# Kernel optimization log

Hardware: AMD Instinct MI355X
Metric: run time of the kernel (lower is better)

## Reference

```python
import jax, jax.numpy as jnp
import numpy as np

N_HEADS = 16
ROPE_BASE = 10000.0


def _rope_cos_sin(seq_len, head_dim, dtype):
    half = head_dim // 2
    inv_freq = 1.0 / (ROPE_BASE ** (jnp.arange(0, half, dtype=jnp.float32) / half))
    ang = jnp.arange(seq_len, dtype=jnp.float32)[:, None] * inv_freq[None, :]  # [S, half]
    cos = jnp.concatenate([jnp.cos(ang), jnp.cos(ang)], axis=-1).astype(dtype)  # [S, hd]
    sin = jnp.concatenate([jnp.sin(ang), jnp.sin(ang)], axis=-1).astype(dtype)
    return cos, sin


def _rotate_half(x):
    half = x.shape[-1] // 2
    return jnp.concatenate([-x[..., half:], x[..., :half]], axis=-1)


def setup_inputs() -> dict:
    key = jax.random.key(0)
    k1, k2, k3 = jax.random.split(key, 3)
    B, S, D = 2, 2048, 1024
    x = jax.random.normal(k1, (B, S, D), dtype=jnp.float32)
    w_qkv = jax.random.normal(k2, (D, 3 * D), dtype=jnp.float32) * (1.0 / np.sqrt(D))
    w_out = jax.random.normal(k3, (D, D), dtype=jnp.float32) * (1.0 / np.sqrt(D))
    return {"x": x, "w_qkv": w_qkv, "w_out": w_out}


def reference(x, w_qkv, w_out):
    B, S, D = x.shape
    H = N_HEADS
    hd = D // H
    scale = 1.0 / np.sqrt(hd)

    qkv = x @ w_qkv  # [B, S, 3D]
    q, k, v = jnp.split(qkv, 3, axis=-1)
    # [B, H, S, hd]
    q = q.reshape(B, S, H, hd).transpose(0, 2, 1, 3)
    k = k.reshape(B, S, H, hd).transpose(0, 2, 1, 3)
    v = v.reshape(B, S, H, hd).transpose(0, 2, 1, 3)

    cos, sin = _rope_cos_sin(S, hd, x.dtype)  # [S, hd]
    q = q * cos + _rotate_half(q) * sin
    k = k * cos + _rotate_half(k) * sin

    scores = jnp.einsum("bhqd,bhkd->bhqk", q, k) * scale  # [B, H, S, S]
    causal = jnp.tril(jnp.ones((S, S), dtype=bool))
    scores = jnp.where(causal[None, None, :, :], scores, -jnp.inf)

    probs = jax.nn.softmax(scores.astype(jnp.float32), axis=-1).astype(q.dtype)
    out = jnp.einsum("bhqk,bhkd->bhqd", probs, v)  # [B, H, S, hd]
    out = out.transpose(0, 2, 1, 3).reshape(B, S, D)
    return out @ w_out
```

## Files before the change

### kernel.cpp

```cpp
#include <hip/hip_runtime.h>
#include <math.h>
#include <type_traits>

#define B_  2
#define S_  2048
#define D_  1024
#define H_  16

typedef short bf16x8 __attribute__((ext_vector_type(8)));
typedef short bf16x4 __attribute__((ext_vector_type(4)));
typedef float f32x4  __attribute__((ext_vector_type(4)));

__device__ __forceinline__ short f2bf(float f) {
    unsigned u = __builtin_bit_cast(unsigned, f);
    u += 0x7FFFu + ((u >> 16) & 1u);
    return (short)(u >> 16);
}
__device__ __forceinline__ float bf2f(short s) {
    unsigned u = ((unsigned)(unsigned short)s) << 16;
    return __builtin_bit_cast(float, u);
}

__device__ __forceinline__ void gload16(const short* g, const void* l) {
    __builtin_amdgcn_global_load_lds(
        (const __attribute__((address_space(1))) void*)g,
        (__attribute__((address_space(3))) void*)l, 16, 0, 0);
}

__device__ __forceinline__ void transpose_body(
    const float* __restrict__ in, short* __restrict__ out, int K, int N,
    int bx, int by, short (*t)[72], int tid)
{
    const int k0 = by * 64, n0 = bx * 64;
    const int r = tid >> 2;
    const int c = (tid & 3) * 16;
    const float* src = in + (size_t)(k0 + r) * N + n0 + c;
#pragma unroll
    for (int i = 0; i < 16; ++i) t[c + i][r] = f2bf(src[i]);
    __syncthreads();
    short* dst = out + (size_t)(n0 + r) * K + k0 + c;
    *(bf16x8*)(dst)     = *(const bf16x8*)&t[r][c];
    *(bf16x8*)(dst + 8) = *(const bf16x8*)&t[r][c + 8];
}

__global__ __launch_bounds__(256) void prep_kernel(
    const float* __restrict__ x, short* __restrict__ Xb,
    const float* __restrict__ w_qkv, short* __restrict__ Wqt,
    const float* __restrict__ w_out, short* __restrict__ Wot,
    float2* __restrict__ tab)
{
    __shared__ short t[64][72];
    const int bid = blockIdx.x;
    const int tid = threadIdx.x;
    if (bid < 2048) {
        int i = (bid * 256 + tid) * 8;
        float4 a = *(const float4*)(x + i);
        float4 b = *(const float4*)(x + i + 4);
        bf16x8 o;
        o[0] = f2bf(a.x); o[1] = f2bf(a.y); o[2] = f2bf(a.z); o[3] = f2bf(a.w);
        o[4] = f2bf(b.x); o[5] = f2bf(b.y); o[6] = f2bf(b.z); o[7] = f2bf(b.w);
        *(bf16x8*)(Xb + i) = o;
    } else if (bid < 2816) {
        int b2 = bid - 2048;
        transpose_body(w_qkv, Wqt, 1024, 3072, b2 % 48, b2 / 48, t, tid);
    } else if (bid < 3072) {
        int b2 = bid - 2816;
        transpose_body(w_out, Wot, 1024, 1024, b2 % 16, b2 / 16, t, tid);
    } else {
        int idx = (bid - 3072) * 256 + tid;
        int j = idx & 31, s = idx >> 5;
        float inv = powf(10000.0f, -(float)j * (1.0f / 32.0f));
        float sn, cs;
        sincosf((float)s * inv, &sn, &cs);
        tab[idx] = make_float2(cs, sn);
    }
}

__global__ __launch_bounds__(256) void gemm_bt_f32(
    const short* __restrict__ A, const short* __restrict__ Bt,
    float* __restrict__ C, int M, int N, int K)
{
    __shared__ short smem[18432];

    const int tid  = threadIdx.x;
    const int wave = tid >> 6, lane = tid & 63;
    const int quad = lane >> 4, l16 = lane & 15;
    const int wm = wave >> 1, wn = wave & 1;

    const int nbx = N >> 6;
    const int cpx = gridDim.x >> 3;
    const int lin = blockIdx.x;
    const int swz = (lin & 7) * cpx + (lin >> 3);
    const int row0 = (swz / nbx) * 128, col0 = (swz % nbx) * 64;

    f32x4 acc[4][2];
#pragma unroll
    for (int mi = 0; mi < 4; ++mi)
#pragma unroll
        for (int ni = 0; ni < 2; ++ni) acc[mi][ni] = (f32x4)0.f;

    const int sr = tid >> 2;
    const int sc = (tid & 3) * 8;
    const short* a0 = A  + (size_t)(row0 + sr) * K + sc;
    const short* a1 = A  + (size_t)(row0 + 64 + sr) * K + sc;
    const short* b0 = Bt + (size_t)(col0 + sr) * K + sc;

    auto stage = [&](int b, int kt) {
        char* l = (char*)(smem + b * 6144) + wave * 1024;
        const int k0 = kt * 32;
        gload16(a0 + k0, l);
        gload16(a1 + k0, l + 4096);
        gload16(b0 + k0, l + 8192);
    };

    const int NT = K >> 5;
    stage(0, 0);
    stage(1, 1);
    int bufid = 0;
    for (int kt = 0; kt < NT; ++kt) {
        if (kt + 1 < NT) { asm volatile("s_waitcnt vmcnt(3)" ::: "memory"); }
        else             { asm volatile("s_waitcnt vmcnt(0)" ::: "memory"); }
        __builtin_amdgcn_s_barrier();
        __builtin_amdgcn_sched_barrier(0);
        if (kt + 2 < NT) {
            int nb = bufid + 2; if (nb >= 3) nb -= 3;
            stage(nb, kt + 2);
        }

        const short* As = smem + bufid * 6144;
        const short* Bs = As + 4096;
        bf16x8 af[4], bfr[2];
#pragma unroll
        for (int mi = 0; mi < 4; ++mi)
            af[mi] = *(const bf16x8*)(As + (wm * 64 + mi * 16 + l16) * 32 + quad * 8);
#pragma unroll
        for (int ni = 0; ni < 2; ++ni)
            bfr[ni] = *(const bf16x8*)(Bs + (wn * 32 + ni * 16 + l16) * 32 + quad * 8);
#pragma unroll
        for (int mi = 0; mi < 4; ++mi)
#pragma unroll
            for (int ni = 0; ni < 2; ++ni)
                acc[mi][ni] = __builtin_amdgcn_mfma_f32_16x16x32_bf16(
                    af[mi], bfr[ni], acc[mi][ni], 0, 0, 0);

        bufid = (bufid + 1 == 3) ? 0 : bufid + 1;
    }

#pragma unroll
    for (int mi = 0; mi < 4; ++mi)
#pragma unroll
        for (int ni = 0; ni < 2; ++ni)
#pragma unroll
            for (int r = 0; r < 4; ++r) {
                int row = row0 + wm * 64 + mi * 16 + quad * 4 + r;
                int col = col0 + wn * 32 + ni * 16 + l16;
                C[(size_t)row * N + col] = acc[mi][ni][r];
            }
}

__global__ __launch_bounds__(256) void gemm_qkv(
    const short* __restrict__ A, const short* __restrict__ Bt,
    const float2* __restrict__ tab,
    short* __restrict__ Qb, short* __restrict__ Kb, short* __restrict__ Vt)
{
    const int K = 1024;
    extern __shared__ short smem[];
    short* Sc = smem;

    const int tid  = threadIdx.x;
    const int wave = tid >> 6, lane = tid & 63;
    const int quad = lane >> 4, l16 = lane & 15;
    const int wm = wave >> 1, wn = wave & 1;

    const int lin = blockIdx.x;
    const int swz = (lin & 7) * 96 + (lin >> 3);
    const int row0 = (swz / 24) * 128, col0 = (swz % 24) * 128;

    f32x4 acc[4][4];
#pragma unroll
    for (int mi = 0; mi < 4; ++mi)
#pragma unroll
        for (int ni = 0; ni < 4; ++ni) acc[mi][ni] = (f32x4)0.f;

    const int sr = tid >> 2;
    const int sc = (tid & 3) * 8;
    const short* a0 = A  + (size_t)(row0 + sr) * K + sc;
    const short* a1 = A  + (size_t)(row0 + 64 + sr) * K + sc;
    const short* b0 = Bt + (size_t)(col0 + sr) * K + sc;
    const short* b1 = Bt + (size_t)(col0 + 64 + sr) * K + sc;

    auto stage = [&](int b, int kt) {
        char* l = (char*)(smem + b * 8192) + wave * 1024;
        const int k0 = kt * 32;
        gload16(a0 + k0, l);
        gload16(a1 + k0, l + 4096);
        gload16(b0 + k0, l + 8192);
        gload16(b1 + k0, l + 12288);
    };

    const int NT = K >> 5;
    stage(0, 0);
    stage(1, 1);
    int bufid = 0;
    for (int kt = 0; kt < NT; ++kt) {
        if (kt + 1 < NT) { asm volatile("s_waitcnt vmcnt(4)" ::: "memory"); }
        else             { asm volatile("s_waitcnt vmcnt(0)" ::: "memory"); }
        __builtin_amdgcn_s_barrier();
        __builtin_amdgcn_sched_barrier(0);
        if (kt + 2 < NT) {
            int nb = bufid + 2; if (nb >= 3) nb -= 3;
            stage(nb, kt + 2);
        }

        const short* As = smem + bufid * 8192;
        const short* Bs = As + 4096;
        bf16x8 af[4], bfr[4];
#pragma unroll
        for (int mi = 0; mi < 4; ++mi)
            af[mi] = *(const bf16x8*)(As + (wm * 64 + mi * 16 + l16) * 32 + quad * 8);
#pragma unroll
        for (int ni = 0; ni < 4; ++ni)
            bfr[ni] = *(const bf16x8*)(Bs + (wn * 64 + ni * 16 + l16) * 32 + quad * 8);
#pragma unroll
        for (int mi = 0; mi < 4; ++mi)
#pragma unroll
            for (int ni = 0; ni < 4; ++ni)
                acc[mi][ni] = __builtin_amdgcn_mfma_f32_16x16x32_bf16(
                    af[mi], bfr[ni], acc[mi][ni], 0, 0, 0);

        bufid = (bufid + 1 == 3) ? 0 : bufid + 1;
    }

    __syncthreads();

    const int sec  = (col0 + wn * 64) >> 6;
    const int h    = sec & 15;
    const int kind = sec >> 4;
    short* myS = Sc + wave * 4608;

    const int mrow0 = row0 + wm * 64;
    const int b  = mrow0 >> 11;
    const int bh = b * 16 + h;
    const int sbase = mrow0 & (S_ - 1);

    if (kind < 2) {
#pragma unroll
        for (int mi = 0; mi < 4; ++mi) {
#pragma unroll
            for (int r = 0; r < 4; ++r) {
                int sl = mi * 16 + quad * 4 + r;
                int s = sbase + sl;
#pragma unroll
                for (int ni = 0; ni < 2; ++ni) {
                    int j = ni * 16 + l16;
                    float2 t = tab[s * 32 + j];
                    float lo = acc[mi][ni][r], hi = acc[mi][ni + 2][r];
                    float olo = lo * t.x - hi * t.y;
                    float ohi = hi * t.x + lo * t.y;
                    if (kind == 0) { olo *= 0.125f; ohi *= 0.125f; }
                    myS[sl * 72 + j]      = f2bf(olo);
                    myS[sl * 72 + 32 + j] = f2bf(ohi);
                }
            }
        }
        const int rl = lane >> 3;
        const int cl = (lane & 7) * 8;
        short* dst = (kind == 0 ? Qb : Kb);
#pragma unroll
        for (int p = 0; p < 8; ++p) {
            int rr = p * 8 + rl;
            bf16x8 v = *(const bf16x8*)&myS[rr * 72 + cl];
            *(bf16x8*)(dst + ((size_t)bh * S_ + sbase + rr) * 64 + cl) = v;
        }
    } else {
#pragma unroll
        for (int mi = 0; mi < 4; ++mi)
#pragma unroll
            for (int ni = 0; ni < 4; ++ni) {
                bf16x4 p;
                p[0] = f2bf(acc[mi][ni][0]);
                p[1] = f2bf(acc[mi][ni][1]);
                p[2] = f2bf(acc[mi][ni][2]);
                p[3] = f2bf(acc[mi][ni][3]);
                *(bf16x4*)&myS[(ni * 16 + l16) * 72 + mi * 16 + quad * 4] = p;
            }
        const int rl = lane >> 3;
        const int cl = (lane & 7) * 8;
#pragma unroll
        for (int p = 0; p < 8; ++p) {
            int dd = p * 8 + rl;
            bf16x8 v = *(const bf16x8*)&myS[dd * 72 + cl];
            *(bf16x8*)(Vt + ((size_t)bh * 64 + dd) * S_ + sbase + cl) = v;
        }
    }
}

__global__ __launch_bounds__(256, 3) void attn_kernel(
    const short* __restrict__ Qb, const short* __restrict__ Kb,
    const short* __restrict__ Vt, short* __restrict__ Opart,
    float* __restrict__ lpart)
{
    __shared__ short Ks[2][64 * 64];
    __shared__ short Vs[2][64 * 64];
    __shared__ short Ps[128][72];

    const int lin = blockIdx.x;
    const int xcd = lin & 7;
    const int j   = lin >> 3;
    const int bh   = xcd * 4 + (j & 3);
    const int task = j >> 2;

    const int g = task < 4 ? 0 : task < 12 ? 1 : task < 24 ? 2 : 3;
    const int cumstart = g == 0 ? 0 : g == 1 ? 4 : g == 2 ? 12 : 24;
    const int idx = task - cumstart;
    const int qd = idx / (g + 1);
    const int qb = 4 * g + qd;
    const int c  = idx - qd * (g + 1);
    const int t0 = c * 8;
    const int t1 = min(2 * qb + 1, c * 8 + 7);

    const int wave = threadIdx.x >> 6, lane = threadIdx.x & 63;
    const int quad = lane >> 4, l16 = lane & 15;
    const int subr  = lane >> 3;
    const int chunk = (lane & 7) ^ subr;
    const size_t head64 = (size_t)bh * S_ * 64;

    bf16x8 qf[2][2];
#pragma unroll
    for (int m = 0; m < 2; ++m) {
        const short* qrow = Qb + head64
            + (size_t)(qb * 128 + wave * 32 + m * 16 + l16) * 64 + quad * 8;
        qf[m][0] = *(const bf16x8*)(qrow);
        qf[m][1] = *(const bf16x8*)(qrow + 32);
    }

    bf16x8 ones;
#pragma unroll
    for (int i = 0; i < 8; ++i) ones[i] = (short)0x3F80;

    auto stage = [&](int buf, int t) {
        const short* kt = Kb + head64 + (size_t)(t * 64 + wave * 16) * 64;
        const short* vt = Vt + head64 + (size_t)(wave * 16) * S_ + t * 64;
        char* kl = (char*)(Ks[buf]) + wave * 2048;
        char* vl = (char*)(Vs[buf]) + wave * 2048;
#pragma unroll
        for (int g2 = 0; g2 < 2; ++g2) {
            gload16(kt + (g2 * 8 + subr) * 64 + chunk * 8, kl + g2 * 1024);
            gload16(vt + (size_t)(g2 * 8 + subr) * S_ + chunk * 8, vl + g2 * 1024);
        }
    };

    f32x4 lacc[2] = {(f32x4)0.f, (f32x4)0.f};
    f32x4 oacc[2][4];
#pragma unroll
    for (int m = 0; m < 2; ++m)
#pragma unroll
        for (int nt = 0; nt < 4; ++nt) oacc[m][nt] = (f32x4)0.f;

    stage(0, t0);
    int buf = 0;
    for (int t = t0; t <= t1; ++t) {
        __builtin_amdgcn_s_barrier();
        if (t < t1) stage(buf ^ 1, t + 1);
        if (t < t1) { asm volatile("s_waitcnt vmcnt(4)" ::: "memory"); }
        else        { asm volatile("s_waitcnt vmcnt(0)" ::: "memory"); }
        __builtin_amdgcn_s_barrier();
        __builtin_amdgcn_sched_barrier(0);

        const short* kbuf = Ks[buf];
        const short* vbuf = Vs[buf];

        f32x4 s4[2][4];
        __builtin_amdgcn_s_setprio(1);
#pragma unroll
        for (int nt = 0; nt < 4; ++nt) {
            const int krow = nt * 16 + l16;
            const int sw = krow & 7;
            bf16x8 k0 = *(const bf16x8*)(kbuf + krow * 64 + ((quad ^ sw) << 3));
            bf16x8 k1 = *(const bf16x8*)(kbuf + krow * 64 + (((quad + 4) ^ sw) << 3));
#pragma unroll
            for (int m = 0; m < 2; ++m) {
                f32x4 a = (f32x4)0.f;
                a = __builtin_amdgcn_mfma_f32_16x16x32_bf16(k0, qf[m][0], a, 0, 0, 0);
                a = __builtin_amdgcn_mfma_f32_16x16x32_bf16(k1, qf[m][1], a, 0, 0, 0);
                s4[m][nt] = a;
            }
        }
        __builtin_amdgcn_s_setprio(0);

        if (t >= 2 * qb) {
            const int kbase = (t - 2 * qb) * 64;
#pragma unroll
            for (int m = 0; m < 2; ++m) {
                const int qq = wave * 32 + m * 16 + l16;
#pragma unroll
                for (int nt = 0; nt < 4; ++nt)
#pragma unroll
                    for (int r = 0; r < 4; ++r)
                        if (kbase + nt * 16 + quad * 4 + r > qq)
                            s4[m][nt][r] = -INFINITY;
            }
        }

#pragma unroll
        for (int m = 0; m < 2; ++m)
#pragma unroll
            for (int nt = 0; nt < 4; ++nt) {
                bf16x4 p;
#pragma unroll
                for (int r = 0; r < 4; ++r)
                    p[r] = f2bf(__expf(s4[m][nt][r] - 8.0f));
                *(bf16x4*)&Ps[wave * 32 + m * 16 + l16][nt * 16 + quad * 4] = p;
            }

        bf16x8 pa[2][2];
#pragma unroll
        for (int m = 0; m < 2; ++m) {
            pa[m][0] = *(const bf16x8*)&Ps[wave * 32 + m * 16 + l16][quad * 8];
            pa[m][1] = *(const bf16x8*)&Ps[wave * 32 + m * 16 + l16][32 + quad * 8];
        }

        __builtin_amdgcn_s_setprio(1);
#pragma unroll
        for (int m = 0; m < 2; ++m) {
            lacc[m] = __builtin_amdgcn_mfma_f32_16x16x32_bf16(pa[m][0], ones, lacc[m], 0, 0, 0);
            lacc[m] = __builtin_amdgcn_mfma_f32_16x16x32_bf16(pa[m][1], ones, lacc[m], 0, 0, 0);
        }
#pragma unroll
        for (int nt = 0; nt < 4; ++nt) {
            const int vrow = nt * 16 + l16;
            const int sw = vrow & 7;
            bf16x8 v0 = *(const bf16x8*)(vbuf + vrow * 64 + ((quad ^ sw) << 3));
            bf16x8 v1 = *(const bf16x8*)(vbuf + vrow * 64 + (((quad + 4) ^ sw) << 3));
#pragma unroll
            for (int m = 0; m < 2; ++m) {
                oacc[m][nt] = __builtin_amdgcn_mfma_f32_16x16x32_bf16(
                    pa[m][0], v0, oacc[m][nt], 0, 0, 0);
                oacc[m][nt] = __builtin_amdgcn_mfma_f32_16x16x32_bf16(
                    pa[m][1], v1, oacc[m][nt], 0, 0, 0);
            }
        }
        __builtin_amdgcn_s_setprio(0);
        buf ^= 1;
    }

    const int pidx = bh * 40 + task;
#pragma unroll
    for (int m = 0; m < 2; ++m)
#pragma unroll
        for (int r = 0; r < 4; ++r) {
            int ql = wave * 32 + m * 16 + quad * 4 + r;
            short* orow = Opart + (size_t)pidx * 8192 + ql * 64;
#pragma unroll
            for (int nt = 0; nt < 4; ++nt)
                orow[nt * 16 + l16] = f2bf(oacc[m][nt][r]);
            if (l16 == 0)
                lpart[(size_t)pidx * 128 + ql] = lacc[m][r];
        }
}

__global__ __launch_bounds__(256) void combine_kernel(
    const short* __restrict__ Opart, const float* __restrict__ lpart,
    short* __restrict__ attnb)
{
    const int qb = blockIdx.x, bh = blockIdx.y;
    const int g = qb >> 2, nch = g + 1;
    const int cumstart = g == 0 ? 0 : g == 1 ? 4 : g == 2 ? 12 : 24;
    const int cbase = bh * 40 + cumstart + (qb - 4 * g) * nch;
    const int q = threadIdx.x >> 1;
    const int dg = (threadIdx.x & 1) * 32;

    float lsum = 0.f;
    float acc[32];
#pragma unroll
    for (int i = 0; i < 32; ++i) acc[i] = 0.f;

    for (int cc = 0; cc < nch; ++cc) {
        lsum += lpart[(size_t)(cbase + cc) * 128 + q];
        const short* src = Opart + (size_t)(cbase + cc) * 8192 + q * 64 + dg;
#pragma unroll
        for (int w = 0; w < 4; ++w) {
            bf16x8 o = *(const bf16x8*)(src + w * 8);
#pragma unroll
            for (int i = 0; i < 8; ++i) acc[w * 8 + i] += bf2f(o[i]);
        }
    }
    float inv = 1.0f / lsum;
    const int b = bh >> 4, h = bh & 15;
    short* dst = attnb + (size_t)(b * S_ + qb * 128 + q) * 1024 + h * 64 + dg;
#pragma unroll
    for (int w = 0; w < 4; ++w) {
        bf16x8 r;
#pragma unroll
        for (int i = 0; i < 8; ++i) r[i] = f2bf(acc[w * 8 + i] * inv);
        *(bf16x8*)(dst + w * 8) = r;
    }
}

extern "C" void kernel_launch(void* const* d_in, const int* in_sizes, int n_in,
                              void* d_out, int out_size, void* d_ws, size_t ws_size,
                              hipStream_t stream)
{
    const float* x     = (const float*)d_in[0];
    const float* w_qkv = (const float*)d_in[1];
    const float* w_out = (const float*)d_in[2];
    float* out = (float*)d_out;

    short* Qb   = (short*)d_ws;
    short* Kb   = Qb   + (size_t)4096 * 1024;
    short* Vt   = Kb   + (size_t)4096 * 1024;
    short* Xb   = Vt   + (size_t)4096 * 1024;
    short* Wqt  = Xb   + (size_t)4096 * 1024;
    short* Wot  = Wqt  + (size_t)3072 * 1024;
    float2* tab = (float2*)(Wot + (size_t)1024 * 1024);
    short* Opart = (short*)(tab + 2048 * 32);
    float* lbuf  = (float*)(Opart + (size_t)1280 * 8192);
    short* attnb = Xb;

    prep_kernel<<<3328, 256, 0, stream>>>(x, Xb, w_qkv, Wqt, w_out, Wot, tab);

    gemm_qkv<<<768, 256, 49152, stream>>>(Xb, Wqt, tab, Qb, Kb, Vt);

    attn_kernel<<<1280, 256, 0, stream>>>(Qb, Kb, Vt, Opart, lbuf);

    combine_kernel<<<dim3(16, 32), 256, 0, stream>>>(Opart, lbuf, attnb);

    gemm_bt_f32<<<512, 256, 0, stream>>>(attnb, Wot, out, 4096, 1024, 1024);
}
```

Baseline: 175.6 us.

## XOR-swizzle GEMM LDS tiles and drop block-index swizzle in both GEMMs

Both GEMM kernels now permute which 16-byte K-chunk each thread fetches from global memory into LDS, using an XOR of the chunk index with row bits. The fragment reads apply the matching XOR so each lane still gets the right data. The aim is to spread the LDS fragment reads across banks and cut bank conflicts. The block-index swizzle that grouped tiles for L2 locality is also removed in favour of plain row-major tile ordering, which may lower cache reuse.

```diff
diff --git a/kernel.cpp b/kernel.cpp
--- a/kernel.cpp
+++ b/kernel.cpp
@@ -86,12 +86,10 @@
     const int wave = tid >> 6, lane = tid & 63;
     const int quad = lane >> 4, l16 = lane & 15;
     const int wm = wave >> 1, wn = wave & 1;
+    const int rq = quad ^ ((l16 >> 1) & 3);
 
     const int nbx = N >> 6;
-    const int cpx = gridDim.x >> 3;
-    const int lin = blockIdx.x;
-    const int swz = (lin & 7) * cpx + (lin >> 3);
-    const int row0 = (swz / nbx) * 128, col0 = (swz % nbx) * 64;
+    const int row0 = (blockIdx.x / nbx) * 128, col0 = (blockIdx.x % nbx) * 64;
 
     f32x4 acc[4][2];
 #pragma unroll
@@ -100,10 +98,10 @@
         for (int ni = 0; ni < 2; ++ni) acc[mi][ni] = (f32x4)0.f;
 
     const int sr = tid >> 2;
-    const int sc = (tid & 3) * 8;
-    const short* a0 = A  + (size_t)(row0 + sr) * K + sc;
-    const short* a1 = A  + (size_t)(row0 + 64 + sr) * K + sc;
-    const short* b0 = Bt + (size_t)(col0 + sr) * K + sc;
+    const int scs = ((tid & 3) ^ ((tid >> 3) & 3)) * 8;
+    const short* a0 = A  + (size_t)(row0 + sr) * K + scs;
+    const short* a1 = A  + (size_t)(row0 + 64 + sr) * K + scs;
+    const short* b0 = Bt + (size_t)(col0 + sr) * K + scs;
 
     auto stage = [&](int b, int kt) {
         char* l = (char*)(smem + b * 6144) + wave * 1024;
@@ -132,10 +130,10 @@
         bf16x8 af[4], bfr[2];
 #pragma unroll
         for (int mi = 0; mi < 4; ++mi)
-            af[mi] = *(const bf16x8*)(As + (wm * 64 + mi * 16 + l16) * 32 + quad * 8);
+            af[mi] = *(const bf16x8*)(As + (wm * 64 + mi * 16 + l16) * 32 + rq * 8);
 #pragma unroll
         for (int ni = 0; ni < 2; ++ni)
-            bfr[ni] = *(const bf16x8*)(Bs + (wn * 32 + ni * 16 + l16) * 32 + quad * 8);
+            bfr[ni] = *(const bf16x8*)(Bs + (wn * 32 + ni * 16 + l16) * 32 + rq * 8);
 #pragma unroll
         for (int mi = 0; mi < 4; ++mi)
 #pragma unroll
@@ -171,10 +169,9 @@
     const int wave = tid >> 6, lane = tid & 63;
     const int quad = lane >> 4, l16 = lane & 15;
     const int wm = wave >> 1, wn = wave & 1;
-
-    const int lin = blockIdx.x;
-    const int swz = (lin & 7) * 96 + (lin >> 3);
-    const int row0 = (swz / 24) * 128, col0 = (swz % 24) * 128;
+    const int rq = quad ^ ((l16 >> 1) & 3);
+
+    const int row0 = (blockIdx.x / 24) * 128, col0 = (blockIdx.x % 24) * 128;
 
     f32x4 acc[4][4];
 #pragma unroll
@@ -183,11 +180,11 @@
         for (int ni = 0; ni < 4; ++ni) acc[mi][ni] = (f32x4)0.f;
 
     const int sr = tid >> 2;
-    const int sc = (tid & 3) * 8;
-    const short* a0 = A  + (size_t)(row0 + sr) * K + sc;
-    const short* a1 = A  + (size_t)(row0 + 64 + sr) * K + sc;
-    const short* b0 = Bt + (size_t)(col0 + sr) * K + sc;
-    const short* b1 = Bt + (size_t)(col0 + 64 + sr) * K + sc;
+    const int scs = ((tid & 3) ^ ((tid >> 3) & 3)) * 8;
+    const short* a0 = A  + (size_t)(row0 + sr) * K + scs;
+    const short* a1 = A  + (size_t)(row0 + 64 + sr) * K + scs;
+    const short* b0 = Bt + (size_t)(col0 + sr) * K + scs;
+    const short* b1 = Bt + (size_t)(col0 + 64 + sr) * K + scs;
 
     auto stage = [&](int b, int kt) {
         char* l = (char*)(smem + b * 8192) + wave * 1024;
@@ -217,10 +214,10 @@
         bf16x8 af[4], bfr[4];
 #pragma unroll
         for (int mi = 0; mi < 4; ++mi)
-            af[mi] = *(const bf16x8*)(As + (wm * 64 + mi * 16 + l16) * 32 + quad * 8);
+            af[mi] = *(const bf16x8*)(As + (wm * 64 + mi * 16 + l16) * 32 + rq * 8);
 #pragma unroll
         for (int ni = 0; ni < 4; ++ni)
-            bfr[ni] = *(const bf16x8*)(Bs + (wn * 64 + ni * 16 + l16) * 32 + quad * 8);
+            bfr[ni] = *(const bf16x8*)(Bs + (wn * 64 + ni * 16 + l16) * 32 + rq * 8);
 #pragma unroll
         for (int mi = 0; mi < 4; ++mi)
 #pragma unroll
```

Measured after the change: 176.0 us. Within noise of the previous version (+0.2%).

## Drop split-KV attention and combine kernel; one block per query tile

Applied to the files above, without the earlier changes.

Replaces the split-KV attention (1280 blocks writing partial outputs and row sums, then a combine kernel) with 512 blocks that each process the whole causal KV range for one 128-row query tile. Tiles are ordered longest first, and each block normalizes its own output and writes it directly through LDS. It also removes the XCD-aware block swizzles from both GEMMs. This removes the partial-output traffic and one kernel launch, at the cost of fewer, unequal-length blocks that may leave CUs idle at the tail and poorer L2 locality in the GEMMs.

```diff
diff --git a/kernel.cpp b/kernel.cpp
--- a/kernel.cpp
+++ b/kernel.cpp
@@ -88,10 +88,7 @@
     const int wm = wave >> 1, wn = wave & 1;
 
     const int nbx = N >> 6;
-    const int cpx = gridDim.x >> 3;
-    const int lin = blockIdx.x;
-    const int swz = (lin & 7) * cpx + (lin >> 3);
-    const int row0 = (swz / nbx) * 128, col0 = (swz % nbx) * 64;
+    const int row0 = (blockIdx.x / nbx) * 128, col0 = (blockIdx.x % nbx) * 64;
 
     f32x4 acc[4][2];
 #pragma unroll
@@ -172,9 +169,7 @@
     const int quad = lane >> 4, l16 = lane & 15;
     const int wm = wave >> 1, wn = wave & 1;
 
-    const int lin = blockIdx.x;
-    const int swz = (lin & 7) * 96 + (lin >> 3);
-    const int row0 = (swz / 24) * 128, col0 = (swz % 24) * 128;
+    const int row0 = (blockIdx.x / 24) * 128, col0 = (blockIdx.x % 24) * 128;
 
     f32x4 acc[4][4];
 #pragma unroll
@@ -297,8 +292,7 @@
 
 __global__ __launch_bounds__(256, 3) void attn_kernel(
     const short* __restrict__ Qb, const short* __restrict__ Kb,
-    const short* __restrict__ Vt, short* __restrict__ Opart,
-    float* __restrict__ lpart)
+    const short* __restrict__ Vt, short* __restrict__ attnb)
 {
     __shared__ short Ks[2][64 * 64];
     __shared__ short Vs[2][64 * 64];
@@ -306,18 +300,11 @@
 
     const int lin = blockIdx.x;
     const int xcd = lin & 7;
-    const int j   = lin >> 3;
-    const int bh   = xcd * 4 + (j & 3);
-    const int task = j >> 2;
-
-    const int g = task < 4 ? 0 : task < 12 ? 1 : task < 24 ? 2 : 3;
-    const int cumstart = g == 0 ? 0 : g == 1 ? 4 : g == 2 ? 12 : 24;
-    const int idx = task - cumstart;
-    const int qd = idx / (g + 1);
-    const int qb = 4 * g + qd;
-    const int c  = idx - qd * (g + 1);
-    const int t0 = c * 8;
-    const int t1 = min(2 * qb + 1, c * 8 + 7);
+    const int bh  = xcd * 4 + ((lin >> 3) & 3);
+    const int m_  = lin >> 5;
+    const int qb  = m_ < 8 ? 15 - m_ : m_ - 8;
+
+    const int t1 = 2 * qb + 1;
 
     const int wave = threadIdx.x >> 6, lane = threadIdx.x & 63;
     const int quad = lane >> 4, l16 = lane & 15;
@@ -357,9 +344,9 @@
 #pragma unroll
         for (int nt = 0; nt < 4; ++nt) oacc[m][nt] = (f32x4)0.f;
 
-    stage(0, t0);
+    stage(0, 0);
     int buf = 0;
-    for (int t = t0; t <= t1; ++t) {
+    for (int t = 0; t <= t1; ++t) {
         __builtin_amdgcn_s_barrier();
         if (t < t1) stage(buf ^ 1, t + 1);
         if (t < t1) { asm volatile("s_waitcnt vmcnt(4)" ::: "memory"); }
@@ -444,56 +431,24 @@
         buf ^= 1;
     }
 
-    const int pidx = bh * 40 + task;
 #pragma unroll
     for (int m = 0; m < 2; ++m)
 #pragma unroll
         for (int r = 0; r < 4; ++r) {
-            int ql = wave * 32 + m * 16 + quad * 4 + r;
-            short* orow = Opart + (size_t)pidx * 8192 + ql * 64;
+            float inv = 1.0f / lacc[m][r];
+            int row = wave * 32 + m * 16 + quad * 4 + r;
 #pragma unroll
             for (int nt = 0; nt < 4; ++nt)
-                orow[nt * 16 + l16] = f2bf(oacc[m][nt][r]);
-            if (l16 == 0)
-                lpart[(size_t)pidx * 128 + ql] = lacc[m][r];
-        }
-}
-
-__global__ __launch_bounds__(256) void combine_kernel(
-    const short* __restrict__ Opart, const float* __restrict__ lpart,
-    short* __restrict__ attnb)
-{
-    const int qb = blockIdx.x, bh = blockIdx.y;
-    const int g = qb >> 2, nch = g + 1;
-    const int cumstart = g == 0 ? 0 : g == 1 ? 4 : g == 2 ? 12 : 24;
-    const int cbase = bh * 40 + cumstart + (qb - 4 * g) * nch;
-    const int q = threadIdx.x >> 1;
-    const int dg = (threadIdx.x & 1) * 32;
-
-    float lsum = 0.f;
-    float acc[32];
-#pragma unroll
-    for (int i = 0; i < 32; ++i) acc[i] = 0.f;
-
-    for (int cc = 0; cc < nch; ++cc) {
-        lsum += lpart[(size_t)(cbase + cc) * 128 + q];
-        const short* src = Opart + (size_t)(cbase + cc) * 8192 + q * 64 + dg;
-#pragma unroll
-        for (int w = 0; w < 4; ++w) {
-            bf16x8 o = *(const bf16x8*)(src + w * 8);
-#pragma unroll
-            for (int i = 0; i < 8; ++i) acc[w * 8 + i] += bf2f(o[i]);
-        }
-    }
-    float inv = 1.0f / lsum;
-    const int b = bh >> 4, h = bh & 15;
-    short* dst = attnb + (size_t)(b * S_ + qb * 128 + q) * 1024 + h * 64 + dg;
-#pragma unroll
-    for (int w = 0; w < 4; ++w) {
-        bf16x8 r;
-#pragma unroll
-        for (int i = 0; i < 8; ++i) r[i] = f2bf(acc[w * 8 + i] * inv);
-        *(bf16x8*)(dst + w * 8) = r;
+                Ps[row][nt * 16 + l16] = f2bf(oacc[m][nt][r] * inv);
+        }
+    const int bb = bh >> 4, h = bh & 15;
+    const int rl = lane >> 3, cl = (lane & 7) * 8;
+#pragma unroll
+    for (int p = 0; p < 4; ++p) {
+        int rr = wave * 32 + p * 8 + rl;
+        bf16x8 v = *(const bf16x8*)&Ps[rr][cl];
+        *(bf16x8*)(attnb + ((size_t)(bb * S_ + qb * 128 + rr)) * 1024
+                   + h * 64 + cl) = v;
     }
 }
 
@@ -513,17 +468,13 @@
     short* Wqt  = Xb   + (size_t)4096 * 1024;
     short* Wot  = Wqt  + (size_t)3072 * 1024;
     float2* tab = (float2*)(Wot + (size_t)1024 * 1024);
-    short* Opart = (short*)(tab + 2048 * 32);
-    float* lbuf  = (float*)(Opart + (size_t)1280 * 8192);
     short* attnb = Xb;
 
     prep_kernel<<<3328, 256, 0, stream>>>(x, Xb, w_qkv, Wqt, w_out, Wot, tab);
 
     gemm_qkv<<<768, 256, 49152, stream>>>(Xb, Wqt, tab, Qb, Kb, Vt);
 
-    attn_kernel<<<1280, 256, 0, stream>>>(Qb, Kb, Vt, Opart, lbuf);
-
-    combine_kernel<<<dim3(16, 32), 256, 0, stream>>>(Opart, lbuf, attnb);
+    attn_kernel<<<512, 256, 0, stream>>>(Qb, Kb, Vt, attnb);
 
     gemm_bt_f32<<<512, 256, 0, stream>>>(attnb, Wot, out, 4096, 1024, 1024);
 }
```

Result: no change. 178.3 us (+1.5%).
